# Kernel optimization log

Measured on AMD Instinct MI355X. Metric: run time of the kernel, lower is better.

## Reference

```python
import jax, jax.numpy as jnp
import numpy as np

B, N, D = 2048, 64, 128
LRELU_ALPHA = 0.2
STEP = 2
NEG_BIG = -9e15


def _leaky(x):
    return jnp.where(x >= 0, x, LRELU_ALPHA * x)


def _local_agg(h, adj, a_list):
    # Original builds a_input[b,i,j,:] = h[b,i,:]*h[b,j,:] (O(N^2*D) buffer)
    # then e_k = leakyrelu(a_input @ a_k).  Mathematically e_k[b,i,j] =
    # leakyrelu(sum_d h[b,i,d]*a_k[d]*h[b,j,d]) = bilinear score, computed
    # here directly as a batched GEMM (same math, no N^2*D intermediate).
    logits = jnp.full(h.shape[:2] + (h.shape[1],), NEG_BIG, dtype=h.dtype)
    for k, a in enumerate(a_list):
        e_k = _leaky(jnp.einsum('bid,bjd->bij', h * a[:, 0], h))
        logits = jnp.where(adj == (k + 1), e_k, logits)
    att = jax.nn.softmax(logits, axis=-1)          # [B,N,N]
    return att @ h                                  # [B,N,D]


def setup_inputs() -> dict:
    key = jax.random.key(0)
    ks = jax.random.split(key, 13)
    hidden = jax.random.normal(ks[0], (B, N, D), dtype=jnp.float32)
    adj = jax.random.randint(ks[1], (B, N, N), 0, 5, dtype=jnp.int32)
    mask = (jax.random.uniform(ks[2], (B, N)) < 0.8).astype(jnp.float32)
    mask = mask.at[:, 0].set(1.0)  # guarantee at least one valid node per session
    s = 1.0 / np.sqrt(D)
    mk = lambda i, shp: (jax.random.normal(ks[i], shp, dtype=jnp.float32) * s)
    return {
        'hidden': hidden, 'adj': adj, 'mask': mask,
        'a_0': mk(3, (D, 1)), 'a_1': mk(4, (D, 1)),
        'a_2': mk(5, (D, 1)), 'a_3': mk(6, (D, 1)),
        'q_1': mk(7, (D, D)), 'k_1': mk(8, (D, D)),
        'q_2': mk(9, (D, D)), 'k_2': mk(10, (D, D)),
        'W_lin': mk(11, (D, 2 * D)),  # torch Linear(2D -> D, no bias) weight
    }


def reference(hidden, adj, mask, a_0, a_1, a_2, a_3,
              q_1, k_1, q_2, k_2, W_lin):
    sqrt_d = jnp.sqrt(jnp.asarray(D, hidden.dtype))
    # star init: masked mean over nodes -> [B,1,D]
    avg = jnp.sum(hidden * mask[..., None], axis=1) / jnp.sum(mask, axis=1, keepdims=True)
    star = avg[:, None, :]
    sate = hidden
    a_list = (a_0, a_1, a_2, a_3)
    for _ in range(STEP):
        sate = _local_agg(sate, adj, a_list)
        # satellite -> star attention (scalar gate per node)
        q = sate @ q_1                               # [B,N,D]
        k = star @ k_1                               # [B,1,D]
        alpha = (q @ jnp.swapaxes(k, -2, -1)) / sqrt_d  # [B,N,1]
        sate = (1.0 - alpha) * sate + alpha * star
        # star update: masked attention over satellites
        q2 = star @ q_2                              # [B,1,D]
        k2 = sate @ k_2                              # [B,N,D]
        beta = (q2 @ jnp.swapaxes(k2, -2, -1)) / sqrt_d  # [B,1,N]
        beta = jnp.where(mask[:, None, :] == 0, -jnp.inf, beta)
        beta = jax.nn.softmax(beta, axis=-1)
        star = beta @ sate                           # [B,1,D]
    gate = jax.nn.sigmoid(jnp.concatenate([hidden, sate], axis=-1) @ W_lin.T)
    out = gate * hidden + (1.0 - gate) * sate
    return out, star
```

## Files before the change

kernel.cpp:

```cpp
#include <hip/hip_runtime.h>

#define BDIM 256
constexpr int Bc = 2048;
constexpr int Nc = 64;
constexpr int Dc = 128;
constexpr float NEG_BIG_F = -9.0e15f;
constexpr float INV_SQRT_D = 0.08838834764831845f;

typedef __attribute__((ext_vector_type(8))) short bf16x8;
typedef __attribute__((ext_vector_type(4))) float f32x4;

#define MFMA16(A, B, C) __builtin_amdgcn_mfma_f32_16x16x32_bf16((A), (B), (C), 0, 0, 0)

__device__ __forceinline__ float bf2f(ushort u) {
    union { float f; unsigned int i; } cv;
    cv.i = ((unsigned int)u) << 16;
    return cv.f;
}
__device__ __forceinline__ ushort f2bf(float f) {
    union { float f; unsigned int i; } cv;
    cv.f = f;
    unsigned int x = cv.i;
    unsigned int r = (x >> 16) & 1u;
    x += 0x7fffu + r;
    return (ushort)(x >> 16);
}
__device__ __forceinline__ float rmax16(float v) {
#pragma unroll
    for (int off = 1; off < 16; off <<= 1) v = fmaxf(v, __shfl_xor(v, off, 64));
    return v;
}
__device__ __forceinline__ float rsum16(float v) {
#pragma unroll
    for (int off = 1; off < 16; off <<= 1) v += __shfl_xor(v, off, 64);
    return v;
}

__global__ __launch_bounds__(BDIM, 3) void star_agg_kernel(
    const float* __restrict__ hid,
    const int*   __restrict__ adj,
    const float* __restrict__ maskp,
    const float* __restrict__ a0p, const float* __restrict__ a1p,
    const float* __restrict__ a2p, const float* __restrict__ a3p,
    const float* __restrict__ q1p, const float* __restrict__ k1p,
    const float* __restrict__ q2p, const float* __restrict__ k2p,
    const float* __restrict__ wlp,
    float* __restrict__ outp)
{
    __shared__ __align__(16) ushort hb[Nc][136];
    __shared__ __align__(16) ushort hlo[Nc][136];
    __shared__ __align__(16) ushort Pb[Nc][72];
    __shared__ float aL[4][Dc];
    __shared__ float star_s[Dc];
    __shared__ float kk_s[Dc], qq_s[Dc];
    __shared__ float vv_s[Dc], ww_s[Dc];
    __shared__ float m_s[Nc];
    __shared__ float beta_s[Nc];
    __shared__ float star_part[4][Dc];

    const int b      = blockIdx.x;
    const int tid    = threadIdx.x;
    const int lane   = tid & 63;
    const int wv     = tid >> 6;
    const int lane15 = lane & 15;
    const int quad   = lane >> 4;

    {
        const float4* hp4 = (const float4*)(hid + (size_t)b * (Nc * Dc));
        for (int idx = tid; idx < (Nc * Dc) / 4; idx += BDIM) {
            const int r = idx >> 5;
            const int c = (idx & 31) * 4;
            const float4 v = hp4[idx];
            ushort4 hi4, lo4;
            hi4.x = f2bf(v.x); lo4.x = f2bf(v.x - bf2f(hi4.x));
            hi4.y = f2bf(v.y); lo4.y = f2bf(v.y - bf2f(hi4.y));
            hi4.z = f2bf(v.z); lo4.z = f2bf(v.z - bf2f(hi4.z));
            hi4.w = f2bf(v.w); lo4.w = f2bf(v.w - bf2f(hi4.w));
            *(ushort4*)&hb[r][c]  = hi4;
            *(ushort4*)&hlo[r][c] = lo4;
        }
        if (tid < 128) {
            const int t = tid >> 5, c4 = tid & 31;
            const float* ap = (t == 0) ? a0p : (t == 1) ? a1p : (t == 2) ? a2p : a3p;
            *(float4*)&aL[t][c4 * 4] = *(const float4*)&ap[c4 * 4];
        }
        if (tid < Nc) m_s[tid] = maskp[b * Nc + tid];
    }
    __syncthreads();

    if (tid < Dc) {
        float s = 0.f, ms = 0.f;
        for (int i = 0; i < Nc; ++i) {
            const float hv = bf2f(hb[i][tid]) + bf2f(hlo[i][tid]);
            s = fmaf(hv, m_s[i], s);
            ms += m_s[i];
        }
        star_s[tid] = s / ms;
    }
    __syncthreads();

    float s2[8][4];

    for (int step = 0; step < 2; ++step) {
        if (tid < Dc) {
            const int c = tid;
            float s = 0.f;
            for (int d = 0; d < Dc; ++d) s = fmaf(star_s[d], k1p[d * Dc + c], s);
            kk_s[c] = s;
        } else {
            const int c = tid - Dc;
            float s = 0.f;
            for (int d = 0; d < Dc; ++d) s = fmaf(star_s[d], q2p[d * Dc + c], s);
            qq_s[c] = s;
        }
        __syncthreads();
        if (tid < Dc) {
            const int c = tid;
            float s = 0.f;
            for (int e4 = 0; e4 < Dc; e4 += 4) {
                const float4 qv = *(const float4*)&q1p[c * Dc + e4];
                s = fmaf(qv.w, kk_s[e4 + 3], fmaf(qv.z, kk_s[e4 + 2],
                    fmaf(qv.y, kk_s[e4 + 1], fmaf(qv.x, kk_s[e4], s))));
            }
            vv_s[c] = s * INV_SQRT_D;
        } else {
            const int c = tid - Dc;
            float s = 0.f;
            for (int e4 = 0; e4 < Dc; e4 += 4) {
                const float4 kv = *(const float4*)&k2p[c * Dc + e4];
                s = fmaf(kv.w, qq_s[e4 + 3], fmaf(kv.z, qq_s[e4 + 2],
                    fmaf(kv.y, qq_s[e4 + 1], fmaf(kv.x, qq_s[e4], s))));
            }
            ww_s[c] = s * INV_SQRT_D;
        }
        __syncthreads();

        f32x4 eacc[4][4];
#pragma unroll
        for (int t = 0; t < 4; ++t)
#pragma unroll
            for (int n = 0; n < 4; ++n) eacc[t][n] = (f32x4)0.f;

        const int arow = wv * 16 + lane15;
#pragma unroll
        for (int kc = 0; kc < 4; ++kc) {
            const int ko = kc * 32 + quad * 8;
            const bf16x8 hh = *(const bf16x8*)&hb[arow][ko];
            const bf16x8 hl = *(const bf16x8*)&hlo[arow][ko];
            float hx[8];
#pragma unroll
            for (int e = 0; e < 8; ++e)
                hx[e] = bf2f((ushort)hh[e]) + bf2f((ushort)hl[e]);
            bf16x8 Ahi[4], Alo[4];
#pragma unroll
            for (int t = 0; t < 4; ++t) {
                const float4 a0 = *(const float4*)&aL[t][ko];
                const float4 a1 = *(const float4*)&aL[t][ko + 4];
                const float av[8] = {a0.x, a0.y, a0.z, a0.w, a1.x, a1.y, a1.z, a1.w};
#pragma unroll
                for (int e = 0; e < 8; ++e) {
                    const float p = hx[e] * av[e];
                    const ushort ph = f2bf(p);
                    const ushort pl = f2bf(p - bf2f(ph));
                    Ahi[t][e] = (short)ph;
                    Alo[t][e] = (short)pl;
                }
            }
#pragma unroll
            for (int n = 0; n < 4; ++n) {
                const int brow = n * 16 + lane15;
                const bf16x8 Bh = *(const bf16x8*)&hb[brow][ko];
                const bf16x8 Bl = *(const bf16x8*)&hlo[brow][ko];
#pragma unroll
                for (int t = 0; t < 4; ++t) {
                    eacc[t][n] = MFMA16(Ahi[t], Bh, eacc[t][n]);
                    eacc[t][n] = MFMA16(Ahi[t], Bl, eacc[t][n]);
                    eacc[t][n] = MFMA16(Alo[t], Bh, eacc[t][n]);
                }
            }
        }

        float lg[4][4];
#pragma unroll
        for (int n = 0; n < 4; ++n) {
#pragma unroll
            for (int r = 0; r < 4; ++r) {
                const int i = wv * 16 + quad * 4 + r;
                const int j = n * 16 + lane15;
                const int t = adj[(size_t)b * 4096 + i * 64 + j];
                const float v0 = eacc[0][n][r], v1 = eacc[1][n][r];
                const float v2 = eacc[2][n][r], v3 = eacc[3][n][r];
                const float sel = (t == 1) ? v0 : (t == 2) ? v1 : (t == 3) ? v2 : v3;
                const float e = (t >= 1 && t <= 4) ? ((sel >= 0.f) ? sel : 0.2f * sel)
                                                   : NEG_BIG_F;
                lg[n][r] = e;
            }
        }

#pragma unroll
        for (int r = 0; r < 4; ++r) {
            float mx = fmaxf(fmaxf(lg[0][r], lg[1][r]), fmaxf(lg[2][r], lg[3][r]));
            mx = rmax16(mx);
            float pr[4], s = 0.f;
#pragma unroll
            for (int n = 0; n < 4; ++n) { pr[n] = __expf(lg[n][r] - mx); s += pr[n]; }
            s = rsum16(s);
            const float inv = 1.f / s;
            const int irow = wv * 16 + quad * 4 + r;
#pragma unroll
            for (int n = 0; n < 4; ++n)
                Pb[irow][n * 16 + lane15] = f2bf(pr[n] * inv);
        }
        __syncthreads();

        f32x4 s1[8];
#pragma unroll
        for (int nd = 0; nd < 8; ++nd) s1[nd] = (f32x4)0.f;
#pragma unroll
        for (int kc2 = 0; kc2 < 2; ++kc2) {
            const int ko = kc2 * 32 + quad * 8;
            const bf16x8 Pa = *(const bf16x8*)&Pb[wv * 16 + lane15][ko];
#pragma unroll
            for (int nd = 0; nd < 8; ++nd) {
                const int dc = nd * 16 + lane15;
                bf16x8 Bf;
#pragma unroll
                for (int jj = 0; jj < 8; ++jj) Bf[jj] = (short)hb[ko + jj][dc];
                s1[nd] = MFMA16(Pa, Bf, s1[nd]);
            }
        }

        float vvv[8], stv[8];
#pragma unroll
        for (int nt = 0; nt < 8; ++nt) {
            vvv[nt] = vv_s[nt * 16 + lane15];
            stv[nt] = star_s[nt * 16 + lane15];
        }
#pragma unroll
        for (int r = 0; r < 4; ++r) {
            float part = 0.f;
#pragma unroll
            for (int nt = 0; nt < 8; ++nt) part = fmaf(s1[nt][r], vvv[nt], part);
            const float al = rsum16(part);
#pragma unroll
            for (int nt = 0; nt < 8; ++nt)
                s2[nt][r] = (1.f - al) * s1[nt][r] + al * stv[nt];
        }

        float www[8];
#pragma unroll
        for (int nt = 0; nt < 8; ++nt) www[nt] = ww_s[nt * 16 + lane15];
        float bm[4];
#pragma unroll
        for (int r = 0; r < 4; ++r) {
            float part = 0.f;
#pragma unroll
            for (int nt = 0; nt < 8; ++nt) part = fmaf(s2[nt][r], www[nt], part);
            const float bj = rsum16(part);
            const int j = wv * 16 + quad * 4 + r;
            bm[r] = (m_s[j] == 0.f) ? NEG_BIG_F : bj;
            if (lane15 == 0) beta_s[j] = bm[r];
        }
        __syncthreads();

        {
            float mx = NEG_BIG_F;
#pragma unroll
            for (int j4 = 0; j4 < 16; ++j4) {
                const float4 bv = *(const float4*)&beta_s[j4 * 4];
                mx = fmaxf(mx, fmaxf(fmaxf(bv.x, bv.y), fmaxf(bv.z, bv.w)));
            }
            float p[4];
#pragma unroll
            for (int r = 0; r < 4; ++r) p[r] = __expf(bm[r] - mx);
            float part[8];
#pragma unroll
            for (int nt = 0; nt < 8; ++nt) {
                float v = 0.f;
#pragma unroll
                for (int r = 0; r < 4; ++r) v = fmaf(p[r], s2[nt][r], v);
                v += __shfl_xor(v, 16, 64);
                v += __shfl_xor(v, 32, 64);
                part[nt] = v;
            }
            if (lane < 16) {
#pragma unroll
                for (int nt = 0; nt < 8; ++nt)
                    star_part[wv][nt * 16 + lane15] = part[nt];
            }
#pragma unroll
            for (int nt = 0; nt < 8; ++nt) {
#pragma unroll
                for (int r = 0; r < 4; ++r) {
                    const float v = s2[nt][r];
                    const ushort hi = f2bf(v);
                    const ushort lo = f2bf(v - bf2f(hi));
                    const int row = wv * 16 + quad * 4 + r;
                    const int c   = nt * 16 + lane15;
                    hb[row][c]  = hi;
                    hlo[row][c] = lo;
                }
            }
        }
        __syncthreads();
        if (tid < Dc) {
            float mx = NEG_BIG_F;
            for (int j = 0; j < Nc; ++j) mx = fmaxf(mx, beta_s[j]);
            float S = 0.f;
            for (int j = 0; j < Nc; ++j) S += __expf(beta_s[j] - mx);
            const float tot = star_part[0][tid] + star_part[1][tid]
                            + star_part[2][tid] + star_part[3][tid];
            star_s[tid] = tot / S;
        }
        __syncthreads();
    }

    f32x4 g[8];
#pragma unroll
    for (int n = 0; n < 8; ++n) g[n] = (f32x4)0.f;
    const int arow_g = wv * 16 + lane15;
    const float* hrowA = hid + ((size_t)b * 64 + arow_g) * Dc;
#pragma unroll
    for (int kc = 0; kc < 8; ++kc) {
        bf16x8 Ah, Al;
        const bool has_lo = (kc >= 4);
        if (!has_lo) {
            const int co = kc * 32 + quad * 8;
            const float4 h0 = *(const float4*)&hrowA[co];
            const float4 h1 = *(const float4*)&hrowA[co + 4];
            const float hv[8] = {h0.x, h0.y, h0.z, h0.w, h1.x, h1.y, h1.z, h1.w};
#pragma unroll
            for (int e = 0; e < 8; ++e) Ah[e] = (short)f2bf(hv[e]);
        } else {
            const int co = (kc - 4) * 32 + quad * 8;
            Ah = *(const bf16x8*)&hb[arow_g][co];
            Al = *(const bf16x8*)&hlo[arow_g][co];
        }
#pragma unroll
        for (int n = 0; n < 8; ++n) {
            const int orow = n * 16 + lane15;
            const float* wr = wlp + orow * 256 + kc * 32 + quad * 8;
            const float4 w0 = *(const float4*)&wr[0];
            const float4 w1 = *(const float4*)&wr[4];
            const float wvv[8] = {w0.x, w0.y, w0.z, w0.w, w1.x, w1.y, w1.z, w1.w};
            bf16x8 Bf;
#pragma unroll
            for (int e = 0; e < 8; ++e) Bf[e] = (short)f2bf(wvv[e]);
            g[n] = MFMA16(Ah, Bf, g[n]);
            if (has_lo) g[n] = MFMA16(Al, Bf, g[n]);
        }
    }

#pragma unroll
    for (int n = 0; n < 8; ++n) {
#pragma unroll
        for (int r = 0; r < 4; ++r) {
            const int i = wv * 16 + quad * 4 + r;
            const int o = n * 16 + lane15;
            const float gg = 1.f / (1.f + __expf(-g[n][r]));
            const float hv = hid[((size_t)b * 64 + i) * Dc + o];
            outp[((size_t)b * 64 + i) * Dc + o] = gg * hv + (1.f - gg) * s2[n][r];
        }
    }
    if (tid < Dc)
        outp[(size_t)Bc * Nc * Dc + (size_t)b * Dc + tid] = star_s[tid];
}

extern "C" void kernel_launch(void* const* d_in, const int* in_sizes, int n_in,
                              void* d_out, int out_size, void* d_ws, size_t ws_size,
                              hipStream_t stream) {
    const float* hid  = (const float*)d_in[0];
    const int*   adj  = (const int*)d_in[1];
    const float* mask = (const float*)d_in[2];
    const float* a0   = (const float*)d_in[3];
    const float* a1   = (const float*)d_in[4];
    const float* a2   = (const float*)d_in[5];
    const float* a3   = (const float*)d_in[6];
    const float* q1   = (const float*)d_in[7];
    const float* k1   = (const float*)d_in[8];
    const float* q2   = (const float*)d_in[9];
    const float* k2   = (const float*)d_in[10];
    const float* wl   = (const float*)d_in[11];
    float* out = (float*)d_out;

    star_agg_kernel<<<Bc, BDIM, 0, stream>>>(hid, adj, mask, a0, a1, a2, a3,
                                             q1, k1, q2, k2, wl, out);
}
```

Before: 504.2 us.

## Precompute fused weight matrices, swizzle LDS layout, prefetch adjacency, pre-convert gate weights

Adds a prep kernel that multiplies the q1/k1 and k2/q2 pairs into single 128x128 matrices and converts W_lin to bf16 once per call, so each block does one matvec per step instead of two chained ones. The h tiles in LDS get an XOR swizzle to cut bank conflicts, and adjacency types are loaded up front into packed registers. Pb and the star partials now share one LDS union, and a barrier between them is removed. The changes trade an extra launch and a different weight-product rounding order for less per-block work; the union aliasing without a barrier is a correctness risk.

```diff
diff --git a/kernel.cpp b/kernel.cpp
--- a/kernel.cpp
+++ b/kernel.cpp
@@ -36,6 +36,40 @@
     return v;
 }
 
+__global__ void prep_kernel(const float* __restrict__ q1p, const float* __restrict__ k1p,
+                            const float* __restrict__ q2p, const float* __restrict__ k2p,
+                            const float* __restrict__ wlp,
+                            float* __restrict__ M1t, float* __restrict__ M2t,
+                            ushort* __restrict__ wbf)
+{
+    const int z   = blockIdx.x;
+    const int tid = threadIdx.x;
+    const bool isM1 = (z < 32);
+    const int zz = isM1 ? z : z - 32;
+    const float* Arow = isM1 ? q1p : k2p;
+    const float* Brow = isM1 ? k1p : q2p;
+    float* Mt = isM1 ? M1t : M2t;
+    const int c = tid & 127;
+#pragma unroll
+    for (int dd = 0; dd < 2; ++dd) {
+        const int d = zz * 4 + ((tid >> 7) << 1) + dd;
+        float s = 0.f;
+#pragma unroll 8
+        for (int e = 0; e < Dc; e += 4) {
+            const float4 av = *(const float4*)&Arow[c * Dc + e];
+            const float4 bv = *(const float4*)&Brow[d * Dc + e];
+            s = fmaf(av.w, bv.w, fmaf(av.z, bv.z, fmaf(av.y, bv.y, fmaf(av.x, bv.x, s))));
+        }
+        Mt[d * Dc + c] = s * INV_SQRT_D;
+    }
+#pragma unroll
+    for (int k = 0; k < 2; ++k) {
+        const int i = (z * 256 + tid) * 2 + k;
+        wbf[i] = f2bf(wlp[i]);
+    }
+}
+
+template <int HAS_WS>
 __global__ __launch_bounds__(BDIM, 3) void star_agg_kernel(
     const float* __restrict__ hid,
     const int*   __restrict__ adj,
@@ -45,18 +79,19 @@
     const float* __restrict__ q1p, const float* __restrict__ k1p,
     const float* __restrict__ q2p, const float* __restrict__ k2p,
     const float* __restrict__ wlp,
+    const float* __restrict__ M1t, const float* __restrict__ M2t,
+    const ushort* __restrict__ wbf,
     float* __restrict__ outp)
 {
     __shared__ __align__(16) ushort hb[Nc][136];
     __shared__ __align__(16) ushort hlo[Nc][136];
-    __shared__ __align__(16) ushort Pb[Nc][72];
+    union PbU { ushort Pb[Nc][72]; float part[4][Dc]; };
+    __shared__ __align__(16) PbU PU;
     __shared__ float aL[4][Dc];
     __shared__ float star_s[Dc];
-    __shared__ float kk_s[Dc], qq_s[Dc];
     __shared__ float vv_s[Dc], ww_s[Dc];
     __shared__ float m_s[Nc];
     __shared__ float beta_s[Nc];
-    __shared__ float star_part[4][Dc];
 
     const int b      = blockIdx.x;
     const int tid    = threadIdx.x;
@@ -70,14 +105,15 @@
         for (int idx = tid; idx < (Nc * Dc) / 4; idx += BDIM) {
             const int r = idx >> 5;
             const int c = (idx & 31) * 4;
+            const int pc = ((((c >> 3) ^ (r >> 3)) & 15) << 3) + (c & 7);
             const float4 v = hp4[idx];
             ushort4 hi4, lo4;
             hi4.x = f2bf(v.x); lo4.x = f2bf(v.x - bf2f(hi4.x));
             hi4.y = f2bf(v.y); lo4.y = f2bf(v.y - bf2f(hi4.y));
             hi4.z = f2bf(v.z); lo4.z = f2bf(v.z - bf2f(hi4.z));
             hi4.w = f2bf(v.w); lo4.w = f2bf(v.w - bf2f(hi4.w));
-            *(ushort4*)&hb[r][c]  = hi4;
-            *(ushort4*)&hlo[r][c] = lo4;
+            *(ushort4*)&hb[r][pc]  = hi4;
+            *(ushort4*)&hlo[r][pc] = lo4;
         }
         if (tid < 128) {
             const int t = tid >> 5, c4 = tid & 31;
@@ -86,12 +122,29 @@
         }
         if (tid < Nc) m_s[tid] = maskp[b * Nc + tid];
     }
+
+    unsigned int apack0 = 0u, apack1 = 0u;
+    {
+        const int* ab = adj + (size_t)b * 4096;
+#pragma unroll
+        for (int n = 0; n < 4; ++n)
+#pragma unroll
+            for (int r = 0; r < 4; ++r) {
+                const int i = wv * 16 + quad * 4 + r;
+                const int j = n * 16 + lane15;
+                const unsigned t = (unsigned)ab[i * 64 + j] & 15u;
+                const int idx = n * 4 + r;
+                if (idx < 8) apack0 |= t << (idx * 4);
+                else         apack1 |= t << ((idx - 8) * 4);
+            }
+    }
     __syncthreads();
 
     if (tid < Dc) {
         float s = 0.f, ms = 0.f;
         for (int i = 0; i < Nc; ++i) {
-            const float hv = bf2f(hb[i][tid]) + bf2f(hlo[i][tid]);
+            const int pc = ((((tid >> 3) ^ (i >> 3)) & 15) << 3) + (tid & 7);
+            const float hv = bf2f(hb[i][pc]) + bf2f(hlo[i][pc]);
             s = fmaf(hv, m_s[i], s);
             ms += m_s[i];
         }
@@ -102,38 +155,55 @@
     float s2[8][4];
 
     for (int step = 0; step < 2; ++step) {
-        if (tid < Dc) {
-            const int c = tid;
-            float s = 0.f;
-            for (int d = 0; d < Dc; ++d) s = fmaf(star_s[d], k1p[d * Dc + c], s);
-            kk_s[c] = s;
+        if (HAS_WS) {
+            const float* Mt = (tid < Dc) ? M1t : M2t;
+            const int c = tid & 127;
+            float a0 = 0.f, a1 = 0.f, a2 = 0.f, a3 = 0.f;
+            for (int d = 0; d < Dc; d += 4) {
+                a0 = fmaf(Mt[(d + 0) * Dc + c], star_s[d + 0], a0);
+                a1 = fmaf(Mt[(d + 1) * Dc + c], star_s[d + 1], a1);
+                a2 = fmaf(Mt[(d + 2) * Dc + c], star_s[d + 2], a2);
+                a3 = fmaf(Mt[(d + 3) * Dc + c], star_s[d + 3], a3);
+            }
+            const float res = (a0 + a1) + (a2 + a3);
+            if (tid < Dc) vv_s[c] = res; else ww_s[c] = res;
+            __syncthreads();
         } else {
-            const int c = tid - Dc;
-            float s = 0.f;
-            for (int d = 0; d < Dc; ++d) s = fmaf(star_s[d], q2p[d * Dc + c], s);
-            qq_s[c] = s;
-        }
-        __syncthreads();
-        if (tid < Dc) {
-            const int c = tid;
-            float s = 0.f;
-            for (int e4 = 0; e4 < Dc; e4 += 4) {
-                const float4 qv = *(const float4*)&q1p[c * Dc + e4];
-                s = fmaf(qv.w, kk_s[e4 + 3], fmaf(qv.z, kk_s[e4 + 2],
-                    fmaf(qv.y, kk_s[e4 + 1], fmaf(qv.x, kk_s[e4], s))));
-            }
-            vv_s[c] = s * INV_SQRT_D;
-        } else {
-            const int c = tid - Dc;
-            float s = 0.f;
-            for (int e4 = 0; e4 < Dc; e4 += 4) {
-                const float4 kv = *(const float4*)&k2p[c * Dc + e4];
-                s = fmaf(kv.w, qq_s[e4 + 3], fmaf(kv.z, qq_s[e4 + 2],
-                    fmaf(kv.y, qq_s[e4 + 1], fmaf(kv.x, qq_s[e4], s))));
-            }
-            ww_s[c] = s * INV_SQRT_D;
-        }
-        __syncthreads();
+            float* kk_s = PU.part[0];
+            float* qq_s = PU.part[1];
+            if (tid < Dc) {
+                const int c = tid;
+                float s = 0.f;
+                for (int d = 0; d < Dc; ++d) s = fmaf(star_s[d], k1p[d * Dc + c], s);
+                kk_s[c] = s;
+            } else {
+                const int c = tid - Dc;
+                float s = 0.f;
+                for (int d = 0; d < Dc; ++d) s = fmaf(star_s[d], q2p[d * Dc + c], s);
+                qq_s[c] = s;
+            }
+            __syncthreads();
+            if (tid < Dc) {
+                const int c = tid;
+                float s = 0.f;
+                for (int e4 = 0; e4 < Dc; e4 += 4) {
+                    const float4 qv = *(const float4*)&q1p[c * Dc + e4];
+                    s = fmaf(qv.w, kk_s[e4 + 3], fmaf(qv.z, kk_s[e4 + 2],
+                        fmaf(qv.y, kk_s[e4 + 1], fmaf(qv.x, kk_s[e4], s))));
+                }
+                vv_s[c] = s * INV_SQRT_D;
+            } else {
+                const int c = tid - Dc;
+                float s = 0.f;
+                for (int e4 = 0; e4 < Dc; e4 += 4) {
+                    const float4 kv = *(const float4*)&k2p[c * Dc + e4];
+                    s = fmaf(kv.w, qq_s[e4 + 3], fmaf(kv.z, qq_s[e4 + 2],
+                        fmaf(kv.y, qq_s[e4 + 1], fmaf(kv.x, qq_s[e4], s))));
+                }
+                ww_s[c] = s * INV_SQRT_D;
+            }
+            __syncthreads();
+        }
 
         f32x4 eacc[4][4];
 #pragma unroll
@@ -142,11 +212,14 @@
             for (int n = 0; n < 4; ++n) eacc[t][n] = (f32x4)0.f;
 
         const int arow = wv * 16 + lane15;
+        const int aswz = arow >> 3;
 #pragma unroll
         for (int kc = 0; kc < 4; ++kc) {
-            const int ko = kc * 32 + quad * 8;
-            const bf16x8 hh = *(const bf16x8*)&hb[arow][ko];
-            const bf16x8 hl = *(const bf16x8*)&hlo[arow][ko];
+            const int ko  = kc * 32 + quad * 8;
+            const int kch = ko >> 3;
+            const int kph = (((kch ^ aswz) & 15) << 3);
+            const bf16x8 hh = *(const bf16x8*)&hb[arow][kph];
+            const bf16x8 hl = *(const bf16x8*)&hlo[arow][kph];
             float hx[8];
 #pragma unroll
             for (int e = 0; e < 8; ++e)
@@ -169,8 +242,9 @@
 #pragma unroll
             for (int n = 0; n < 4; ++n) {
                 const int brow = n * 16 + lane15;
-                const bf16x8 Bh = *(const bf16x8*)&hb[brow][ko];
-                const bf16x8 Bl = *(const bf16x8*)&hlo[brow][ko];
+                const int kbh  = (((kch ^ (brow >> 3)) & 15) << 3);
+                const bf16x8 Bh = *(const bf16x8*)&hb[brow][kbh];
+                const bf16x8 Bl = *(const bf16x8*)&hlo[brow][kbh];
 #pragma unroll
                 for (int t = 0; t < 4; ++t) {
                     eacc[t][n] = MFMA16(Ahi[t], Bh, eacc[t][n]);
@@ -185,9 +259,9 @@
         for (int n = 0; n < 4; ++n) {
 #pragma unroll
             for (int r = 0; r < 4; ++r) {
-                const int i = wv * 16 + quad * 4 + r;
-                const int j = n * 16 + lane15;
-                const int t = adj[(size_t)b * 4096 + i * 64 + j];
+                const int idx = n * 4 + r;
+                const int t = (int)((idx < 8 ? (apack0 >> (idx * 4))
+                                             : (apack1 >> ((idx - 8) * 4))) & 15u);
                 const float v0 = eacc[0][n][r], v1 = eacc[1][n][r];
                 const float v2 = eacc[2][n][r], v3 = eacc[3][n][r];
                 const float sel = (t == 1) ? v0 : (t == 2) ? v1 : (t == 3) ? v2 : v3;
@@ -209,23 +283,24 @@
             const int irow = wv * 16 + quad * 4 + r;
 #pragma unroll
             for (int n = 0; n < 4; ++n)
-                Pb[irow][n * 16 + lane15] = f2bf(pr[n] * inv);
-        }
-        __syncthreads();
+                PU.Pb[irow][n * 16 + lane15] = f2bf(pr[n] * inv);
+        }
 
         f32x4 s1[8];
 #pragma unroll
         for (int nd = 0; nd < 8; ++nd) s1[nd] = (f32x4)0.f;
 #pragma unroll
         for (int kc2 = 0; kc2 < 2; ++kc2) {
-            const int ko = kc2 * 32 + quad * 8;
-            const bf16x8 Pa = *(const bf16x8*)&Pb[wv * 16 + lane15][ko];
+            const int ko   = kc2 * 32 + quad * 8;
+            const int swzr = ko >> 3;
+            const bf16x8 Pa = *(const bf16x8*)&PU.Pb[wv * 16 + lane15][ko];
 #pragma unroll
             for (int nd = 0; nd < 8; ++nd) {
                 const int dc = nd * 16 + lane15;
+                const int pc = ((((dc >> 3) ^ swzr) & 15) << 3) + (dc & 7);
                 bf16x8 Bf;
 #pragma unroll
-                for (int jj = 0; jj < 8; ++jj) Bf[jj] = (short)hb[ko + jj][dc];
+                for (int jj = 0; jj < 8; ++jj) Bf[jj] = (short)hb[ko + jj][pc];
                 s1[nd] = MFMA16(Pa, Bf, s1[nd]);
             }
         }
@@ -286,8 +361,9 @@
             if (lane < 16) {
 #pragma unroll
                 for (int nt = 0; nt < 8; ++nt)
-                    star_part[wv][nt * 16 + lane15] = part[nt];
-            }
+                    PU.part[wv][nt * 16 + lane15] = part[nt];
+            }
+            const int row = wv * 16 + quad * 4;
 #pragma unroll
             for (int nt = 0; nt < 8; ++nt) {
 #pragma unroll
@@ -295,21 +371,31 @@
                     const float v = s2[nt][r];
                     const ushort hi = f2bf(v);
                     const ushort lo = f2bf(v - bf2f(hi));
-                    const int row = wv * 16 + quad * 4 + r;
-                    const int c   = nt * 16 + lane15;
-                    hb[row][c]  = hi;
-                    hlo[row][c] = lo;
+                    const int rr = row + r;
+                    const int c  = nt * 16 + lane15;
+                    const int pc = ((((c >> 3) ^ (rr >> 3)) & 15) << 3) + (c & 7);
+                    hb[rr][pc]  = hi;
+                    hlo[rr][pc] = lo;
                 }
             }
         }
         __syncthreads();
         if (tid < Dc) {
             float mx = NEG_BIG_F;
-            for (int j = 0; j < Nc; ++j) mx = fmaxf(mx, beta_s[j]);
+#pragma unroll
+            for (int j4 = 0; j4 < 16; ++j4) {
+                const float4 bv = *(const float4*)&beta_s[j4 * 4];
+                mx = fmaxf(mx, fmaxf(fmaxf(bv.x, bv.y), fmaxf(bv.z, bv.w)));
+            }
             float S = 0.f;
-            for (int j = 0; j < Nc; ++j) S += __expf(beta_s[j] - mx);
-            const float tot = star_part[0][tid] + star_part[1][tid]
-                            + star_part[2][tid] + star_part[3][tid];
+#pragma unroll
+            for (int j4 = 0; j4 < 16; ++j4) {
+                const float4 bv = *(const float4*)&beta_s[j4 * 4];
+                S += __expf(bv.x - mx) + __expf(bv.y - mx)
+                   + __expf(bv.z - mx) + __expf(bv.w - mx);
+            }
+            const float tot = PU.part[0][tid] + PU.part[1][tid]
+                            + PU.part[2][tid] + PU.part[3][tid];
             star_s[tid] = tot / S;
         }
         __syncthreads();
@@ -319,6 +405,7 @@
 #pragma unroll
     for (int n = 0; n < 8; ++n) g[n] = (f32x4)0.f;
     const int arow_g = wv * 16 + lane15;
+    const int gswz   = arow_g >> 3;
     const float* hrowA = hid + ((size_t)b * 64 + arow_g) * Dc;
 #pragma unroll
     for (int kc = 0; kc < 8; ++kc) {
@@ -332,20 +419,25 @@
 #pragma unroll
             for (int e = 0; e < 8; ++e) Ah[e] = (short)f2bf(hv[e]);
         } else {
-            const int co = (kc - 4) * 32 + quad * 8;
-            Ah = *(const bf16x8*)&hb[arow_g][co];
-            Al = *(const bf16x8*)&hlo[arow_g][co];
+            const int co  = (kc - 4) * 32 + quad * 8;
+            const int pco = ((((co >> 3) ^ gswz) & 15) << 3);
+            Ah = *(const bf16x8*)&hb[arow_g][pco];
+            Al = *(const bf16x8*)&hlo[arow_g][pco];
         }
 #pragma unroll
         for (int n = 0; n < 8; ++n) {
             const int orow = n * 16 + lane15;
-            const float* wr = wlp + orow * 256 + kc * 32 + quad * 8;
-            const float4 w0 = *(const float4*)&wr[0];
-            const float4 w1 = *(const float4*)&wr[4];
-            const float wvv[8] = {w0.x, w0.y, w0.z, w0.w, w1.x, w1.y, w1.z, w1.w};
             bf16x8 Bf;
-#pragma unroll
-            for (int e = 0; e < 8; ++e) Bf[e] = (short)f2bf(wvv[e]);
+            if (HAS_WS) {
+                Bf = *(const bf16x8*)&wbf[orow * 256 + kc * 32 + quad * 8];
+            } else {
+                const float* wr = wlp + orow * 256 + kc * 32 + quad * 8;
+                const float4 w0 = *(const float4*)&wr[0];
+                const float4 w1 = *(const float4*)&wr[4];
+                const float wvv[8] = {w0.x, w0.y, w0.z, w0.w, w1.x, w1.y, w1.z, w1.w};
+#pragma unroll
+                for (int e = 0; e < 8; ++e) Bf[e] = (short)f2bf(wvv[e]);
+            }
             g[n] = MFMA16(Ah, Bf, g[n]);
             if (has_lo) g[n] = MFMA16(Al, Bf, g[n]);
         }
@@ -383,6 +475,20 @@
     const float* wl   = (const float*)d_in[11];
     float* out = (float*)d_out;
 
-    star_agg_kernel<<<Bc, BDIM, 0, stream>>>(hid, adj, mask, a0, a1, a2, a3,
-                                             q1, k1, q2, k2, wl, out);
-}
+    const size_t ws_needed = (size_t)(128 * 128) * 4 * 2
+                           + (size_t)(128 * 256) * 2;
+
+    if (d_ws != nullptr && ws_size >= ws_needed) {
+        float*  M1t = (float*)d_ws;
+        float*  M2t = M1t + 128 * 128;
+        ushort* wbf = (ushort*)(M2t + 128 * 128);
+        prep_kernel<<<64, 256, 0, stream>>>(q1, k1, q2, k2, wl, M1t, M2t, wbf);
+        star_agg_kernel<1><<<Bc, BDIM, 0, stream>>>(hid, adj, mask, a0, a1, a2, a3,
+                                                    q1, k1, q2, k2, wl,
+                                                    M1t, M2t, wbf, out);
+    } else {
+        star_agg_kernel<0><<<Bc, BDIM, 0, stream>>>(hid, adj, mask, a0, a1, a2, a3,
+                                                    q1, k1, q2, k2, wl,
+                                                    nullptr, nullptr, nullptr, out);
+    }
+}
```

Measured after the change: 660.0 us. +30.9%, slower.
